# Kernel optimization log

Hardware: AMD Instinct MI355X
Metric: run time of the kernel (lower is better)

## Reference

```python
import jax, jax.numpy as jnp
import numpy as np

N_STATE = 1280
N_HEAD = 20
HEAD_DIM = 64  # hardcoded in the original module
B = 1          # batch hardcoded to 1 by reshape in qkv_attention
N_CTX = 32
CACHE = 16384


def setup_inputs() -> dict:
    key = jax.random.key(0)
    ks = jax.random.split(key, 11)
    s = 0.02  # param init scale
    return {
        "x": jax.random.normal(ks[0], (B, N_CTX, N_STATE), jnp.float32),
        "self_k_cache": jax.random.normal(ks[1], (B, CACHE, N_STATE), jnp.float32),
        "self_v_cache": jax.random.normal(ks[2], (B, CACHE, N_STATE), jnp.float32),
        "positions": jnp.arange(N_CTX, dtype=jnp.int64) if jax.config.jax_enable_x64 else jnp.arange(N_CTX, dtype=jnp.int32),
        "mask": jnp.zeros((N_CTX, CACHE), jnp.float32),
        # learned parameters (Linear stores weight as [out, in]; y = x @ W.T + b)
        "Wq": jax.random.normal(ks[3], (N_STATE, N_STATE), jnp.float32) * s,
        "bq": jax.random.normal(ks[4], (N_STATE,), jnp.float32) * s,
        "Wk": jax.random.normal(ks[5], (N_STATE, N_STATE), jnp.float32) * s,  # key has no bias
        "Wv": jax.random.normal(ks[6], (N_STATE, N_STATE), jnp.float32) * s,
        "bv": jax.random.normal(ks[7], (N_STATE,), jnp.float32) * s,
        "Wout": jax.random.normal(ks[8], (N_STATE, N_STATE), jnp.float32) * s,
        "bout": jax.random.normal(ks[9], (N_STATE,), jnp.float32) * s,
    }


def reference(x, self_k_cache, self_v_cache, positions, mask,
              Wq, bq, Wk, Wv, bv, Wout, bout):
    scale2 = HEAD_DIM ** -0.5
    # projections
    q = x @ Wq.T + bq          # [B, n_ctx, n_state]
    k = x @ Wk.T               # [B, n_ctx, n_state] (no bias)
    v = x @ Wv.T + bv
    # scatter KV-cache update: self_k_cache[:, positions, :] = k
    kc = self_k_cache.at[:, positions, :].set(k)   # [B, CACHE, n_state]
    vc = self_v_cache.at[:, positions, :].set(v)
    # split heads
    qh = q.reshape(B, N_CTX, N_HEAD, HEAD_DIM).transpose(0, 2, 1, 3)  # [B,H,q,d]
    kh = kc.reshape(B, CACHE, N_HEAD, HEAD_DIM)                        # [B,k,H,d]
    vh = vc.reshape(B, CACHE, N_HEAD, HEAD_DIM)
    # attention: softmax(q k^T * scale2 + mask) v
    qk = jnp.einsum('bhqd,bkhd->bhqk', qh, kh) * scale2 + mask         # [B,H,q,k]
    w = jax.nn.softmax(qk, axis=-1)
    o = jnp.einsum('bhqk,bkhd->bqhd', w, vh).reshape(1, N_CTX, N_HEAD * HEAD_DIM)
    out = o @ Wout.T + bout
    return out, kc, vc
```

## Files before the change

kernel.cpp:

```cpp
#include <hip/hip_runtime.h>
#include <hip/hip_bf16.h>

#define H 20
#define Q 32
#define D 64
#define NSTATE 1280
#define CACHE_N 16384
#define NSPLIT 32
#define KCHUNK (CACHE_N / NSPLIT)
#define TK 64

__device__ __forceinline__ void gemm_body(const float* __restrict__ x,
                                          const float* __restrict__ W,
                                          const float* __restrict__ bias,
                                          float* __restrict__ out,
                                          int c0, int ksplit) {
    __shared__ float xs[64][36];
    __shared__ float ws[64][66];
    const int t = threadIdx.x;
    const int rt = t >> 5;
    const int ct = t & 31;
    float acc[4][2] = {};

    const int kbeg = ksplit * 320;
#pragma unroll 1
    for (int k0 = kbeg; k0 < kbeg + 320; k0 += 64) {
        __syncthreads();
#pragma unroll
        for (int p = 0; p < 2; ++p) {
            int idx = t + p * 256;
            int row = idx >> 4, c4 = idx & 15;
            float4 v4 = *(const float4*)(x + row * NSTATE + k0 + c4 * 4);
            xs[c4 * 4 + 0][row] = v4.x; xs[c4 * 4 + 1][row] = v4.y;
            xs[c4 * 4 + 2][row] = v4.z; xs[c4 * 4 + 3][row] = v4.w;
        }
#pragma unroll
        for (int p = 0; p < 4; ++p) {
            int idx = t + p * 256;
            int c = idx >> 4, c4 = idx & 15;
            float4 v4 = *(const float4*)(W + (long long)(c0 + c) * NSTATE + k0 + c4 * 4);
            ws[c4 * 4 + 0][c] = v4.x; ws[c4 * 4 + 1][c] = v4.y;
            ws[c4 * 4 + 2][c] = v4.z; ws[c4 * 4 + 3][c] = v4.w;
        }
        __syncthreads();
#pragma unroll 8
        for (int kk = 0; kk < 64; ++kk) {
            float4 xv = *(const float4*)&xs[kk][rt * 4];
            float2 wv = *(const float2*)&ws[kk][ct * 2];
            acc[0][0] += xv.x * wv.x; acc[0][1] += xv.x * wv.y;
            acc[1][0] += xv.y * wv.x; acc[1][1] += xv.y * wv.y;
            acc[2][0] += xv.z * wv.x; acc[2][1] += xv.z * wv.y;
            acc[3][0] += xv.w * wv.x; acc[3][1] += xv.w * wv.y;
        }
    }
#pragma unroll
    for (int r = 0; r < 4; ++r) {
        int i = rt * 4 + r;
#pragma unroll
        for (int cc = 0; cc < 2; ++cc) {
            int c = c0 + ct * 2 + cc;
            float val = acc[r][cc];
            if (ksplit == 0 && bias) val += bias[c];
            atomicAdd(&out[i * NSTATE + c], val);
        }
    }
}

__global__ __launch_bounds__(256, 2)
void gemm_qkv(const float* __restrict__ x,
              const float* __restrict__ Wq, const float* __restrict__ bq,
              const float* __restrict__ Wk,
              const float* __restrict__ Wv, const float* __restrict__ bv,
              float* __restrict__ q, float* __restrict__ k, float* __restrict__ v) {
    const int mat = blockIdx.z;
    const float* W; const float* bias; float* out;
    if (mat == 0)      { W = Wq; bias = bq;      out = q; }
    else if (mat == 1) { W = Wk; bias = nullptr; out = k; }
    else               { W = Wv; bias = bv;      out = v; }
    gemm_body(x, W, bias, out, blockIdx.x * 64, blockIdx.y);
}

__global__ __launch_bounds__(256, 2)
void gemm_one(const float* __restrict__ x, const float* __restrict__ W,
              const float* __restrict__ bias, float* __restrict__ out) {
    gemm_body(x, W, bias, out, blockIdx.x * 64, blockIdx.y);
}

__global__ void build_rowmap(const int* __restrict__ pos, int* __restrict__ rowmap) {
    int i = threadIdx.x;
    if (i < Q) rowmap[pos[i]] = i;
}

__global__ __launch_bounds__(256, 2)
void attn_fused(const float* __restrict__ qw,
                const float* __restrict__ kci, const float* __restrict__ vci,
                const float* __restrict__ knew, const float* __restrict__ vnew,
                const int* __restrict__ rowmap, const float* __restrict__ mask,
                float* __restrict__ kc, float* __restrict__ vc,
                float* __restrict__ mpart, float* __restrict__ lpart,
                __hip_bfloat16* __restrict__ opart) {
    const int h  = blockIdx.y;
    const int sp = blockIdx.x;
    const int j_base = sp * KCHUNK;

    __shared__ float qs[D][36];
    __shared__ float ks_[D][66];
    __shared__ float vs[TK][68];
    __shared__ float ps[TK][36];
    __shared__ float m_s[Q], l_s[Q], alpha_s[Q], tmax[Q], tsum[Q];

    const int t = threadIdx.x;
    const int qt = t >> 5;
    const int kt = t & 31;
    const int dt = t & 31;

#pragma unroll
    for (int p = 0; p < 2; ++p) {
        int idx = t + p * 256;
        int i = idx >> 4, c4 = idx & 15;
        float4 v4 = *(const float4*)(qw + i * NSTATE + h * D + c4 * 4);
        const float sc = 0.125f;
        qs[c4 * 4 + 0][i] = v4.x * sc; qs[c4 * 4 + 1][i] = v4.y * sc;
        qs[c4 * 4 + 2][i] = v4.z * sc; qs[c4 * 4 + 3][i] = v4.w * sc;
    }
    if (t < Q) { m_s[t] = -1e30f; l_s[t] = 0.f; }
    float oacc[4][2] = {};
    __syncthreads();

#pragma unroll 1
    for (int tile = 0; tile < KCHUNK / TK; ++tile) {
        const int j0 = j_base + tile * TK;
        __syncthreads();
#pragma unroll
        for (int p = 0; p < 4; ++p) {
            int idx = t + p * 256;
            int row = idx >> 4, c4 = idx & 15;
            long long j = j0 + row;
            int src = rowmap[j];
            const float* kb; const float* vb;
            if (src >= 0) { kb = knew + (long long)src * NSTATE; vb = vnew + (long long)src * NSTATE; }
            else          { kb = kci + j * NSTATE;               vb = vci + j * NSTATE; }
            float4 k4 = *(const float4*)(kb + h * D + c4 * 4);
            float4 v4 = *(const float4*)(vb + h * D + c4 * 4);
            *(float4*)(kc + j * NSTATE + h * D + c4 * 4) = k4;
            *(float4*)(vc + j * NSTATE + h * D + c4 * 4) = v4;
            ks_[c4 * 4 + 0][row] = k4.x; ks_[c4 * 4 + 1][row] = k4.y;
            ks_[c4 * 4 + 2][row] = k4.z; ks_[c4 * 4 + 3][row] = k4.w;
            *(float4*)&vs[row][c4 * 4] = v4;
        }
        __syncthreads();

        float s[4][2] = {};
#pragma unroll 8
        for (int d = 0; d < D; ++d) {
            float4 qv = *(const float4*)&qs[d][qt * 4];
            float2 kv = *(const float2*)&ks_[d][kt * 2];
            s[0][0] += qv.x * kv.x; s[0][1] += qv.x * kv.y;
            s[1][0] += qv.y * kv.x; s[1][1] += qv.y * kv.y;
            s[2][0] += qv.z * kv.x; s[2][1] += qv.z * kv.y;
            s[3][0] += qv.w * kv.x; s[3][1] += qv.w * kv.y;
        }
#pragma unroll
        for (int r = 0; r < 4; ++r) {
            int i = qt * 4 + r;
            float2 mv = *(const float2*)(mask + (long long)i * CACHE_N + j0 + kt * 2);
            s[r][0] += mv.x; s[r][1] += mv.y;
        }
        float rmax[4];
#pragma unroll
        for (int r = 0; r < 4; ++r) rmax[r] = fmaxf(s[r][0], s[r][1]);
#pragma unroll
        for (int off = 16; off >= 1; off >>= 1)
#pragma unroll
            for (int r = 0; r < 4; ++r)
                rmax[r] = fmaxf(rmax[r], __shfl_xor(rmax[r], off, 64));
        if (kt == 0)
#pragma unroll
            for (int r = 0; r < 4; ++r) tmax[qt * 4 + r] = rmax[r];
        __syncthreads();
        if (t < Q) {
            float mo = m_s[t], mn = fmaxf(mo, tmax[t]);
            float a = __expf(mo - mn);
            m_s[t] = mn; alpha_s[t] = a; l_s[t] *= a;
        }
        __syncthreads();
        float pr[4][2], rsum[4];
#pragma unroll
        for (int r = 0; r < 4; ++r) {
            float mn = m_s[qt * 4 + r];
            pr[r][0] = __expf(s[r][0] - mn);
            pr[r][1] = __expf(s[r][1] - mn);
            rsum[r] = pr[r][0] + pr[r][1];
        }
#pragma unroll
        for (int c = 0; c < 2; ++c)
            *(float4*)&ps[kt * 2 + c][qt * 4] =
                make_float4(pr[0][c], pr[1][c], pr[2][c], pr[3][c]);
#pragma unroll
        for (int off = 16; off >= 1; off >>= 1)
#pragma unroll
            for (int r = 0; r < 4; ++r)
                rsum[r] += __shfl_xor(rsum[r], off, 64);
        if (kt == 0)
#pragma unroll
            for (int r = 0; r < 4; ++r) tsum[qt * 4 + r] = rsum[r];
        {
            float a0 = alpha_s[qt * 4 + 0], a1 = alpha_s[qt * 4 + 1];
            float a2 = alpha_s[qt * 4 + 2], a3 = alpha_s[qt * 4 + 3];
            oacc[0][0] *= a0; oacc[0][1] *= a0;
            oacc[1][0] *= a1; oacc[1][1] *= a1;
            oacc[2][0] *= a2; oacc[2][1] *= a2;
            oacc[3][0] *= a3; oacc[3][1] *= a3;
        }
        __syncthreads();
        if (t < Q) l_s[t] += tsum[t];
#pragma unroll 8
        for (int j = 0; j < TK; ++j) {
            float4 pv = *(const float4*)&ps[j][qt * 4];
            float2 vv = *(const float2*)&vs[j][dt * 2];
            oacc[0][0] += pv.x * vv.x; oacc[0][1] += pv.x * vv.y;
            oacc[1][0] += pv.y * vv.x; oacc[1][1] += pv.y * vv.y;
            oacc[2][0] += pv.z * vv.x; oacc[2][1] += pv.z * vv.y;
            oacc[3][0] += pv.w * vv.x; oacc[3][1] += pv.w * vv.y;
        }
    }
    __syncthreads();
    const int pb = (h * NSPLIT + sp) * Q;
    if (t < Q) { mpart[pb + t] = m_s[t]; lpart[pb + t] = l_s[t]; }
#pragma unroll
    for (int r = 0; r < 4; ++r) {
        int i = qt * 4 + r;
        __hip_bfloat16 hx = __float2bfloat16(oacc[r][0]);
        __hip_bfloat16 hy = __float2bfloat16(oacc[r][1]);
        ushort2 u = make_ushort2(*(unsigned short*)&hx, *(unsigned short*)&hy);
        *(ushort2*)((unsigned short*)opart + (size_t)(pb + i) * D + dt * 2) = u;
    }
}

__global__ __launch_bounds__(64)
void attn_combine(const float* __restrict__ mpart, const float* __restrict__ lpart,
                  const __hip_bfloat16* __restrict__ opart, float* __restrict__ oattn) {
    const int i = blockIdx.x;
    const int h = blockIdx.y;
    const int d = threadIdx.x;
    float m[NSPLIT];
    float gm = -1e30f;
#pragma unroll
    for (int s = 0; s < NSPLIT; ++s) {
        m[s] = mpart[(h * NSPLIT + s) * Q + i];
        gm = fmaxf(gm, m[s]);
    }
    float l = 0.f, o = 0.f;
#pragma unroll
    for (int s = 0; s < NSPLIT; ++s) {
        float w = __expf(m[s] - gm);
        l += lpart[(h * NSPLIT + s) * Q + i] * w;
        o += __bfloat162float(opart[(size_t)((h * NSPLIT + s) * Q + i) * D + d]) * w;
    }
    oattn[i * NSTATE + h * D + d] = o / l;
}

extern "C" void kernel_launch(void* const* d_in, const int* in_sizes, int n_in,
                              void* d_out, int out_size, void* d_ws, size_t ws_size,
                              hipStream_t stream) {
    const float* x    = (const float*)d_in[0];
    const float* kci  = (const float*)d_in[1];
    const float* vci  = (const float*)d_in[2];
    const int*   pos  = (const int*)d_in[3];
    const float* mask = (const float*)d_in[4];
    const float* Wq   = (const float*)d_in[5];
    const float* bq   = (const float*)d_in[6];
    const float* Wk   = (const float*)d_in[7];
    const float* Wv   = (const float*)d_in[8];
    const float* bv   = (const float*)d_in[9];
    const float* Wout = (const float*)d_in[10];
    const float* bout = (const float*)d_in[11];

    float* out  = (float*)d_out;
    float* kc   = out + 40960;
    float* vc   = kc + CACHE_N * NSTATE;

    float* ws      = (float*)d_ws;
    float* kws     = ws;
    float* vws     = ws + 40960;
    float* qws     = ws + 81920;
    float* mpart   = ws + 122880;
    float* lpart   = ws + 143360;
    int*   rowmap  = (int*)(ws + 163840);
    __hip_bfloat16* opart = (__hip_bfloat16*)(ws + 180224);
    float* oattn   = qws;

    hipMemsetAsync(ws, 0, 3 * 40960 * sizeof(float), stream);
    hipMemsetAsync(out, 0, 40960 * sizeof(float), stream);
    hipMemsetAsync(rowmap, 0xFF, CACHE_N * sizeof(int), stream);

    build_rowmap<<<1, 64, 0, stream>>>(pos, rowmap);

    gemm_qkv<<<dim3(NSTATE / 64, 4, 3), 256, 0, stream>>>(x, Wq, bq, Wk, Wv, bv, qws, kws, vws);

    attn_fused<<<dim3(NSPLIT, H), 256, 0, stream>>>(qws, kci, vci, kws, vws, rowmap, mask,
                                                    kc, vc, mpart, lpart, opart);

    attn_combine<<<dim3(Q, H), 64, 0, stream>>>(mpart, lpart, opart, oattn);

    gemm_one<<<dim3(NSTATE / 64, 4), 256, 0, stream>>>(oattn, Wout, bout, out);
}
```

Measured before the change: 403.7 us.

## Drop split-K atomics and memsets, double-buffer GEMMs, use nontemporal cache stores

The projection GEMMs now run each output tile over the full K range with register-prefetched double-buffered shared tiles, writing results directly instead of split-K atomicAdd into zeroed buffers. The three memset calls are removed, and rowmap initialization moves into the build_rowmap kernel. KV cache copy-out stores become nontemporal, and the attention kernel's launch bounds ask for higher occupancy. The GEMMs now launch far fewer blocks (20 or 60), so their parallelism drops in exchange for fewer launches and no atomics.

New measurement: 433.6 us. 7.4% more time.

```diff
diff --git a/kernel.cpp b/kernel.cpp
--- a/kernel.cpp
+++ b/kernel.cpp
@@ -10,48 +10,85 @@
 #define KCHUNK (CACHE_N / NSPLIT)
 #define TK 64
 
-__device__ __forceinline__ void gemm_body(const float* __restrict__ x,
-                                          const float* __restrict__ W,
-                                          const float* __restrict__ bias,
-                                          float* __restrict__ out,
-                                          int c0, int ksplit) {
-    __shared__ float xs[64][36];
-    __shared__ float ws[64][66];
-    const int t = threadIdx.x;
+typedef __attribute__((ext_vector_type(4))) float f32x4;
+
+__device__ __forceinline__ void gemm_fullk(const float* __restrict__ x,
+                                           const float* __restrict__ W,
+                                           const float* __restrict__ bias,
+                                           float* __restrict__ out, int c0) {
+    __shared__ float xs[2][64][36];
+    __shared__ float wt[2][64][66];
+    const int t  = threadIdx.x;
     const int rt = t >> 5;
     const int ct = t & 31;
     float acc[4][2] = {};
-
-    const int kbeg = ksplit * 320;
+    float4 px[2], pw[4];
+
+#pragma unroll
+    for (int p = 0; p < 2; ++p) {
+        int idx = t + p * 256, r = idx >> 4, c4 = idx & 15;
+        px[p] = *(const float4*)(x + r * NSTATE + c4 * 4);
+    }
+#pragma unroll
+    for (int p = 0; p < 4; ++p) {
+        int idx = t + p * 256, c = idx >> 4, c4 = idx & 15;
+        pw[p] = *(const float4*)(W + (long long)(c0 + c) * NSTATE + c4 * 4);
+    }
+#pragma unroll
+    for (int p = 0; p < 2; ++p) {
+        int idx = t + p * 256, r = idx >> 4, c4 = idx & 15;
+        xs[0][c4 * 4 + 0][r] = px[p].x; xs[0][c4 * 4 + 1][r] = px[p].y;
+        xs[0][c4 * 4 + 2][r] = px[p].z; xs[0][c4 * 4 + 3][r] = px[p].w;
+    }
+#pragma unroll
+    for (int p = 0; p < 4; ++p) {
+        int idx = t + p * 256, c = idx >> 4, c4 = idx & 15;
+        wt[0][c4 * 4 + 0][c] = pw[p].x; wt[0][c4 * 4 + 1][c] = pw[p].y;
+        wt[0][c4 * 4 + 2][c] = pw[p].z; wt[0][c4 * 4 + 3][c] = pw[p].w;
+    }
+    __syncthreads();
+
 #pragma unroll 1
-    for (int k0 = kbeg; k0 < kbeg + 320; k0 += 64) {
-        __syncthreads();
-#pragma unroll
-        for (int p = 0; p < 2; ++p) {
-            int idx = t + p * 256;
-            int row = idx >> 4, c4 = idx & 15;
-            float4 v4 = *(const float4*)(x + row * NSTATE + k0 + c4 * 4);
-            xs[c4 * 4 + 0][row] = v4.x; xs[c4 * 4 + 1][row] = v4.y;
-            xs[c4 * 4 + 2][row] = v4.z; xs[c4 * 4 + 3][row] = v4.w;
-        }
-#pragma unroll
-        for (int p = 0; p < 4; ++p) {
-            int idx = t + p * 256;
-            int c = idx >> 4, c4 = idx & 15;
-            float4 v4 = *(const float4*)(W + (long long)(c0 + c) * NSTATE + k0 + c4 * 4);
-            ws[c4 * 4 + 0][c] = v4.x; ws[c4 * 4 + 1][c] = v4.y;
-            ws[c4 * 4 + 2][c] = v4.z; ws[c4 * 4 + 3][c] = v4.w;
-        }
-        __syncthreads();
+    for (int kt = 0; kt < NSTATE / 64; ++kt) {
+        const int buf = kt & 1;
+        if (kt + 1 < NSTATE / 64) {
+            const int k0 = (kt + 1) * 64;
+#pragma unroll
+            for (int p = 0; p < 2; ++p) {
+                int idx = t + p * 256, r = idx >> 4, c4 = idx & 15;
+                px[p] = *(const float4*)(x + r * NSTATE + k0 + c4 * 4);
+            }
+#pragma unroll
+            for (int p = 0; p < 4; ++p) {
+                int idx = t + p * 256, c = idx >> 4, c4 = idx & 15;
+                pw[p] = *(const float4*)(W + (long long)(c0 + c) * NSTATE + k0 + c4 * 4);
+            }
+        }
 #pragma unroll 8
         for (int kk = 0; kk < 64; ++kk) {
-            float4 xv = *(const float4*)&xs[kk][rt * 4];
-            float2 wv = *(const float2*)&ws[kk][ct * 2];
+            float4 xv = *(const float4*)&xs[buf][kk][rt * 4];
+            float2 wv = *(const float2*)&wt[buf][kk][ct * 2];
             acc[0][0] += xv.x * wv.x; acc[0][1] += xv.x * wv.y;
             acc[1][0] += xv.y * wv.x; acc[1][1] += xv.y * wv.y;
             acc[2][0] += xv.z * wv.x; acc[2][1] += xv.z * wv.y;
             acc[3][0] += xv.w * wv.x; acc[3][1] += xv.w * wv.y;
         }
+        if (kt + 1 < NSTATE / 64) {
+            const int nb = buf ^ 1;
+#pragma unroll
+            for (int p = 0; p < 2; ++p) {
+                int idx = t + p * 256, r = idx >> 4, c4 = idx & 15;
+                xs[nb][c4 * 4 + 0][r] = px[p].x; xs[nb][c4 * 4 + 1][r] = px[p].y;
+                xs[nb][c4 * 4 + 2][r] = px[p].z; xs[nb][c4 * 4 + 3][r] = px[p].w;
+            }
+#pragma unroll
+            for (int p = 0; p < 4; ++p) {
+                int idx = t + p * 256, c = idx >> 4, c4 = idx & 15;
+                wt[nb][c4 * 4 + 0][c] = pw[p].x; wt[nb][c4 * 4 + 1][c] = pw[p].y;
+                wt[nb][c4 * 4 + 2][c] = pw[p].z; wt[nb][c4 * 4 + 3][c] = pw[p].w;
+            }
+        }
+        __syncthreads();
     }
 #pragma unroll
     for (int r = 0; r < 4; ++r) {
@@ -59,39 +96,39 @@
 #pragma unroll
         for (int cc = 0; cc < 2; ++cc) {
             int c = c0 + ct * 2 + cc;
-            float val = acc[r][cc];
-            if (ksplit == 0 && bias) val += bias[c];
-            atomicAdd(&out[i * NSTATE + c], val);
-        }
-    }
-}
-
-__global__ __launch_bounds__(256, 2)
+            out[i * NSTATE + c] = acc[r][cc] + (bias ? bias[c] : 0.f);
+        }
+    }
+}
+
+__global__ __launch_bounds__(256)
 void gemm_qkv(const float* __restrict__ x,
               const float* __restrict__ Wq, const float* __restrict__ bq,
               const float* __restrict__ Wk,
               const float* __restrict__ Wv, const float* __restrict__ bv,
               float* __restrict__ q, float* __restrict__ k, float* __restrict__ v) {
-    const int mat = blockIdx.z;
+    const int mat = blockIdx.y;
     const float* W; const float* bias; float* out;
     if (mat == 0)      { W = Wq; bias = bq;      out = q; }
     else if (mat == 1) { W = Wk; bias = nullptr; out = k; }
     else               { W = Wv; bias = bv;      out = v; }
-    gemm_body(x, W, bias, out, blockIdx.x * 64, blockIdx.y);
-}
-
-__global__ __launch_bounds__(256, 2)
+    gemm_fullk(x, W, bias, out, blockIdx.x * 64);
+}
+
+__global__ __launch_bounds__(256)
 void gemm_one(const float* __restrict__ x, const float* __restrict__ W,
               const float* __restrict__ bias, float* __restrict__ out) {
-    gemm_body(x, W, bias, out, blockIdx.x * 64, blockIdx.y);
+    gemm_fullk(x, W, bias, out, blockIdx.x * 64);
 }
 
 __global__ void build_rowmap(const int* __restrict__ pos, int* __restrict__ rowmap) {
-    int i = threadIdx.x;
-    if (i < Q) rowmap[pos[i]] = i;
-}
-
-__global__ __launch_bounds__(256, 2)
+    const int t = threadIdx.x;
+    for (int j = t; j < CACHE_N; j += 256) rowmap[j] = -1;
+    __syncthreads();
+    if (t < Q) rowmap[pos[t]] = t;
+}
+
+__global__ __launch_bounds__(256, 3)
 void attn_fused(const float* __restrict__ qw,
                 const float* __restrict__ kci, const float* __restrict__ vci,
                 const float* __restrict__ knew, const float* __restrict__ vnew,
@@ -142,8 +179,8 @@
             else          { kb = kci + j * NSTATE;               vb = vci + j * NSTATE; }
             float4 k4 = *(const float4*)(kb + h * D + c4 * 4);
             float4 v4 = *(const float4*)(vb + h * D + c4 * 4);
-            *(float4*)(kc + j * NSTATE + h * D + c4 * 4) = k4;
-            *(float4*)(vc + j * NSTATE + h * D + c4 * 4) = v4;
+            __builtin_nontemporal_store(*(const f32x4*)&k4, (f32x4*)(kc + j * NSTATE + h * D + c4 * 4));
+            __builtin_nontemporal_store(*(const f32x4*)&v4, (f32x4*)(vc + j * NSTATE + h * D + c4 * 4));
             ks_[c4 * 4 + 0][row] = k4.x; ks_[c4 * 4 + 1][row] = k4.y;
             ks_[c4 * 4 + 2][row] = k4.z; ks_[c4 * 4 + 3][row] = k4.w;
             *(float4*)&vs[row][c4 * 4] = v4;
@@ -290,18 +327,14 @@
     __hip_bfloat16* opart = (__hip_bfloat16*)(ws + 180224);
     float* oattn   = qws;
 
-    hipMemsetAsync(ws, 0, 3 * 40960 * sizeof(float), stream);
-    hipMemsetAsync(out, 0, 40960 * sizeof(float), stream);
-    hipMemsetAsync(rowmap, 0xFF, CACHE_N * sizeof(int), stream);
-
-    build_rowmap<<<1, 64, 0, stream>>>(pos, rowmap);
-
-    gemm_qkv<<<dim3(NSTATE / 64, 4, 3), 256, 0, stream>>>(x, Wq, bq, Wk, Wv, bv, qws, kws, vws);
+    build_rowmap<<<1, 256, 0, stream>>>(pos, rowmap);
+
+    gemm_qkv<<<dim3(NSTATE / 64, 3), 256, 0, stream>>>(x, Wq, bq, Wk, Wv, bv, qws, kws, vws);
 
     attn_fused<<<dim3(NSPLIT, H), 256, 0, stream>>>(qws, kci, vci, kws, vws, rowmap, mask,
                                                     kc, vc, mpart, lpart, opart);
 
     attn_combine<<<dim3(Q, H), 64, 0, stream>>>(mpart, lpart, opart, oattn);
 
-    gemm_one<<<dim3(NSTATE / 64, 4), 256, 0, stream>>>(oattn, Wout, bout, out);
-}
+    gemm_one<<<NSTATE / 64, 256, 0, stream>>>(oattn, Wout, bout, out);
+}
```
